# Kernel tuning notes

Hardware: AMD Instinct MI355X
Metric: run time of the kernel (lower is better)

## Reference

```python
import jax, jax.numpy as jnp
import numpy as np

N_NODES = 50000


def _gcn_edges(edge_index, n):
    # add self loops, then symmetric GCN normalization D^-1/2 (A+I) D^-1/2
    loop = jnp.arange(n, dtype=edge_index.dtype)
    src = jnp.concatenate([edge_index[0], loop])
    dst = jnp.concatenate([edge_index[1], loop])
    deg = jax.ops.segment_sum(jnp.ones_like(src, dtype=jnp.float32), dst, num_segments=n)
    dinv = jnp.where(deg > 0, jax.lax.rsqrt(deg), 0.0)
    norm = dinv[src] * dinv[dst]
    return src, dst, norm


def _encoder(x, edge_index, w1, b1, w2, b2, w3, b3, n):
    src, dst, norm = _gcn_edges(edge_index, n)

    def prop(h):
        # sparse spmm: scatter-add of normalized gathered source features
        return jax.ops.segment_sum(h[src] * norm[:, None], dst, num_segments=n)

    def layer(h, w, b):
        # powers [0,1,2]: incrementally apply adjacency, linear per power, concat
        outs, cur = [], h
        for p in range(w.shape[0]):
            if p > 0:
                cur = prop(cur)
            outs.append(cur @ w[p] + b[p])
        return jnp.tanh(jnp.concatenate(outs, axis=-1))

    h = layer(x, w1, b1)
    h = layer(h, w2, b2)
    return layer(h, w3, b3)


def setup_inputs() -> dict:
    key = jax.random.key(0)
    ks = jax.random.split(key, 16)
    n, e, d = N_NODES, 800000, 256
    inp = {
        "x": jax.random.normal(ks[0], (n, d), dtype=jnp.float32),
        "edge_index": jax.random.randint(ks[1], (2, e), 0, n, dtype=jnp.int64),
    }
    dims = [(d, 64), (192, 64), (192, 64)]
    i = 2
    for enc in ("out", "in"):
        for li, (din, dout) in enumerate(dims, start=1):
            s = 1.0 / np.sqrt(din)
            inp[f"w{enc}{li}"] = jax.random.uniform(ks[i], (3, din, dout), jnp.float32, -s, s); i += 1
            inp[f"b{enc}{li}"] = jax.random.uniform(ks[i], (3, dout), jnp.float32, -s, s); i += 1
    return inp


def reference(x, edge_index, wout1, bout1, wout2, bout2, wout3, bout3,
              win1, bin1, win2, bin2, win3, bin3):
    n = x.shape[0]
    zout = _encoder(x, edge_index, wout1, bout1, wout2, bout2, wout3, bout3, n)
    zin = _encoder(x, edge_index[::-1], win1, bin1, win2, bin2, win3, bin3, n)
    return (zout, zin)
```

## Files before the change

### kernel.cpp

```cpp
#include <hip/hip_runtime.h>
#include <hip/hip_bf16.h>

#define NN 50000
#define EE 800000
#define NTILES 782
#define NB 391

typedef __bf16 bf16x8 __attribute__((ext_vector_type(8)));
typedef unsigned short us8 __attribute__((ext_vector_type(8)));
typedef float f32x4 __attribute__((ext_vector_type(4)));

__device__ __forceinline__ unsigned short f2bf(float f) {
  unsigned u = __float_as_uint(f);
  u += 0x7FFFu + ((u >> 16) & 1u);
  return (unsigned short)(u >> 16);
}
__device__ __forceinline__ float bflo(unsigned u) { return __uint_as_float(u << 16); }
__device__ __forceinline__ float bfhi(unsigned u) { return __uint_as_float(u & 0xFFFF0000u); }
__device__ __forceinline__ float bf2f(unsigned short h) { return __uint_as_float(((unsigned)h) << 16); }
__device__ __forceinline__ float fast_tanh(float x) {
  float e = __expf(2.0f * x);
  return 1.0f - 2.0f / (e + 1.0f);
}


__global__ __launch_bounds__(256) void k_hist(const int* __restrict__ ei, int* __restrict__ bCnt) {
  __shared__ int h[2 * NB];
  for (int i = threadIdx.x; i < 2 * NB; i += 256) h[i] = 0;
  __syncthreads();
  int base = blockIdx.x * 2048;
#pragma unroll
  for (int j = 0; j < 8; ++j) {
    int e = base + j * 256 + threadIdx.x;
    if (e < EE) {
      int s = ei[e], d = ei[EE + e];
      atomicAdd(&h[d >> 7], 1);
      atomicAdd(&h[NB + (s >> 7)], 1);
    }
  }
  __syncthreads();
  for (int i = threadIdx.x; i < 2 * NB; i += 256) {
    int c = h[i];
    if (c) atomicAdd(&bCnt[i], c);
  }
}

__global__ __launch_bounds__(512) void k_bscan(const int* __restrict__ bCnt,
                                               int* __restrict__ bOff, int* __restrict__ bCur) {
  __shared__ int sd[512];
  int z = blockIdx.x, t = threadIdx.x;
  sd[t] = (t < NB) ? bCnt[z * NB + t] : 0;
  __syncthreads();
  for (int o = 1; o < 512; o <<= 1) {
    int v = (t >= o) ? sd[t - o] : 0;
    __syncthreads();
    sd[t] += v;
    __syncthreads();
  }
  int ex = (t > 0) ? sd[t - 1] : 0;
  if (t < NB) { bOff[z * (NB + 1) + t] = ex; bCur[z * NB + t] = ex; }
  if (t == NB) bOff[z * (NB + 1) + NB] = ex;
}

__global__ __launch_bounds__(256) void k_scatter(const int* __restrict__ ei,
                                                 int* __restrict__ bCur,
                                                 unsigned* __restrict__ binA,
                                                 unsigned* __restrict__ binB) {
  __shared__ int h[2 * NB];
  for (int i = threadIdx.x; i < 2 * NB; i += 256) h[i] = 0;
  __syncthreads();
  int base = blockIdx.x * 2048;
  int s[8], d[8], la[8], lb[8];
#pragma unroll
  for (int j = 0; j < 8; ++j) {
    int e = base + j * 256 + threadIdx.x;
    d[j] = -1;
    if (e < EE) {
      s[j] = ei[e]; d[j] = ei[EE + e];
      la[j] = atomicAdd(&h[d[j] >> 7], 1);
      lb[j] = atomicAdd(&h[NB + (s[j] >> 7)], 1);
    }
  }
  __syncthreads();
  for (int i = threadIdx.x; i < 2 * NB; i += 256) {
    int c = h[i];
    if (c) h[i] = atomicAdd(&bCur[i], c);
  }
  __syncthreads();
#pragma unroll
  for (int j = 0; j < 8; ++j) {
    if (d[j] >= 0) {
      int pa = h[d[j] >> 7] + la[j];
      binA[pa] = ((unsigned)s[j] << 7) | (unsigned)(d[j] & 127);
      int pb = h[NB + (s[j] >> 7)] + lb[j];
      binB[pb] = ((unsigned)d[j] << 7) | (unsigned)(s[j] & 127);
    }
  }
}

__global__ __launch_bounds__(256) void k_build(const unsigned* __restrict__ binA,
                                               const unsigned* __restrict__ binB,
                                               const int* __restrict__ bOff,
                                               int* __restrict__ rpA, int* __restrict__ rpB,
                                               int* __restrict__ colA, int* __restrict__ colB,
                                               float* __restrict__ dinvA, float* __restrict__ dinvB) {
  int z = blockIdx.y, b = blockIdx.x, t = threadIdx.x;
  const unsigned* bin = z ? binB : binA;
  int* rp = z ? rpB : rpA;
  int* col = z ? colB : colA;
  float* dinv = z ? dinvB : dinvA;

  int e0 = bOff[z * (NB + 1) + b], e1 = bOff[z * (NB + 1) + b + 1];

  __shared__ int cnt[128];
  __shared__ int scn[128];
  __shared__ int cur[128];
  if (t < 128) cnt[t] = 0;
  __syncthreads();
  for (int e = e0 + t; e < e1; e += 256) atomicAdd(&cnt[bin[e] & 127], 1);
  __syncthreads();
  if (t < 128) scn[t] = cnt[t];
  __syncthreads();
  for (int o = 1; o < 128; o <<= 1) {
    int v = (t < 128 && t >= o) ? scn[t - o] : 0;
    __syncthreads();
    if (t < 128) scn[t] += v;
    __syncthreads();
  }
  if (t < 128) {
    int ex = scn[t] - cnt[t];
    cur[t] = ex;
    int node = b * 128 + t;
    if (node <= NN) rp[node] = e0 + ex;
    if (node < NN) dinv[node] = rsqrtf((float)(cnt[t] + 1));
  }
  if (b == 0 && t < 8) col[EE + t] = 0;
  __syncthreads();
  for (int e = e0 + t; e < e1; e += 256) {
    unsigned p = bin[e];
    int pos = e0 + atomicAdd(&cur[p & 127], 1);
    col[pos] = (int)(p >> 7);
  }
}


template<int K, bool F32IN>
__global__ __launch_bounds__(256) void k_gemm(const void* __restrict__ in0, const void* __restrict__ in1,
                                              const float* __restrict__ W0, const float* __restrict__ W1,
                                              const float* __restrict__ dinvA, const float* __restrict__ dinvB,
                                              unsigned short* __restrict__ Z0, unsigned short* __restrict__ Z1) {
  constexpr int KS = K / 32;
  constexpr int KP = K + 8;
  __shared__ unsigned short A_lds[64 * KP];
  __shared__ float dvt[64];

  int z = blockIdx.y;
  const void* Ain = z ? in1 : in0;
  const float* W = z ? W1 : W0;
  const float* dinv = z ? dinvB : dinvA;
  unsigned short* Zo = z ? Z1 : Z0;

  int t = threadIdx.x;
  int lane = t & 63, wv = t >> 6;
  int nloc = lane & 15, quad = lane >> 4;

  bf16x8 b[3][KS];
#pragma unroll
  for (int nt = 0; nt < 3; ++nt) {
    int ncol = wv * 48 + nt * 16 + nloc;
    const float* wp = W + (ncol >> 6) * (K * 64) + (ncol & 63);
#pragma unroll
    for (int ks = 0; ks < KS; ++ks) {
      int kb = ks * 32 + quad * 8;
      us8 u;
#pragma unroll
      for (int i = 0; i < 8; ++i) u[i] = f2bf(wp[(kb + i) * 64]);
      b[nt][ks] = __builtin_bit_cast(bf16x8, u);
    }
  }

  for (int bm = blockIdx.x; bm < NTILES; bm += gridDim.x) {
    int m0 = bm * 64;
    __syncthreads();
    if (t < 64) dvt[t] = (m0 + t < NN) ? dinv[m0 + t] : 0.f;
#pragma unroll
    for (int it = 0; it < KS; ++it) {
      int c = it * 256 + t;
      int row = c / (K / 8);
      int kc  = c % (K / 8);
      int gr = m0 + row;
      us8 val;
      if (F32IN) {
        float4 v0 = make_float4(0, 0, 0, 0), v1 = make_float4(0, 0, 0, 0);
        if (gr < NN) {
          const float* Af = (const float*)Ain + (size_t)gr * K + kc * 8;
          v0 = *(const float4*)(Af);
          v1 = *(const float4*)(Af + 4);
        }
        val[0] = f2bf(v0.x); val[1] = f2bf(v0.y); val[2] = f2bf(v0.z); val[3] = f2bf(v0.w);
        val[4] = f2bf(v1.x); val[5] = f2bf(v1.y); val[6] = f2bf(v1.z); val[7] = f2bf(v1.w);
      } else {
        if (gr < NN) val = *(const us8*)((const unsigned short*)Ain + (size_t)gr * K + kc * 8);
        else         val = (us8)0;
      }
      *(us8*)(&A_lds[row * KP + kc * 8]) = val;
    }
    __syncthreads();

    f32x4 acc[4][3];
#pragma unroll
    for (int mt = 0; mt < 4; ++mt)
#pragma unroll
      for (int nt = 0; nt < 3; ++nt) acc[mt][nt] = (f32x4){0.f, 0.f, 0.f, 0.f};

#pragma unroll
    for (int ks = 0; ks < KS; ++ks) {
      bf16x8 a[4];
#pragma unroll
      for (int mt = 0; mt < 4; ++mt)
        a[mt] = *(const bf16x8*)(&A_lds[(mt * 16 + nloc) * KP + ks * 32 + quad * 8]);
#pragma unroll
      for (int mt = 0; mt < 4; ++mt)
#pragma unroll
        for (int nt = 0; nt < 3; ++nt)
          acc[mt][nt] = __builtin_amdgcn_mfma_f32_16x16x32_bf16(a[mt], b[nt][ks], acc[mt][nt], 0, 0, 0);
    }

#pragma unroll
    for (int mt = 0; mt < 4; ++mt) {
      int rowb = m0 + mt * 16 + quad * 4;
#pragma unroll
      for (int nt = 0; nt < 3; ++nt) {
        int colg = wv * 48 + nt * 16 + nloc;
        bool sc = (wv * 48 + nt * 16) >= 64;
#pragma unroll
        for (int r = 0; r < 4; ++r) {
          int rr = rowb + r;
          float scale = sc ? dvt[mt * 16 + quad * 4 + r] : 1.0f;
          if (rr < NN) Zo[(size_t)rr * 192 + colg] = f2bf(acc[mt][nt][r] * scale);
        }
      }
    }
  }
}


__global__ __launch_bounds__(256) void k_prop1(const unsigned short* __restrict__ Z0,
                                               const unsigned short* __restrict__ Z1,
                                               unsigned short* __restrict__ T0,
                                               unsigned short* __restrict__ T1,
                                               const int* __restrict__ rpA, const int* __restrict__ rpB,
                                               const int* __restrict__ colA, const int* __restrict__ colB,
                                               const float* __restrict__ dinvA, const float* __restrict__ dinvB) {
  int z = blockIdx.y;
  const unsigned short* Z = z ? Z1 : Z0;
  unsigned short* T = z ? T1 : T0;
  const int* rp = z ? rpB : rpA;
  const int* col = z ? colB : colA;
  const float* dinv = z ? dinvB : dinvA;

  int wv = threadIdx.x >> 6, lane = threadIdx.x & 63;
  int v = blockIdx.x * 4 + wv;
  v = __builtin_amdgcn_readfirstlane(v);

  int e0 = rp[v], e1 = rp[v + 1];
  float dv = dinv[v];

  unsigned selfv = ((const unsigned*)(Z + (size_t)v * 192 + 64))[lane];
  float ax = bflo(selfv), ay = bfhi(selfv);

  int e = e0;
  if (e + 8 <= e1) {
    int idx[8];
#pragma unroll
    for (int j = 0; j < 8; ++j) idx[j] = col[e + j];
    e += 8;
    for (; e + 8 <= e1; e += 8) {
      int nidx[8];
#pragma unroll
      for (int j = 0; j < 8; ++j) nidx[j] = col[e + j];
      unsigned pp[8];
#pragma unroll
      for (int j = 0; j < 8; ++j) pp[j] = ((const unsigned*)(Z + (size_t)idx[j] * 192 + 64))[lane];
#pragma unroll
      for (int j = 0; j < 8; ++j) { ax += bflo(pp[j]); ay += bfhi(pp[j]); }
#pragma unroll
      for (int j = 0; j < 8; ++j) idx[j] = nidx[j];
    }
    unsigned pp[8];
#pragma unroll
    for (int j = 0; j < 8; ++j) pp[j] = ((const unsigned*)(Z + (size_t)idx[j] * 192 + 64))[lane];
#pragma unroll
    for (int j = 0; j < 8; ++j) { ax += bflo(pp[j]); ay += bfhi(pp[j]); }
  }
  int r = e1 - e;
  if (r > 0) {
    int idx[8];
#pragma unroll
    for (int j = 0; j < 8; ++j) idx[j] = col[e + j];
    unsigned pp[8];
#pragma unroll
    for (int j = 0; j < 8; ++j) pp[j] = ((const unsigned*)(Z + (size_t)idx[j] * 192 + 64))[lane];
#pragma unroll
    for (int j = 0; j < 8; ++j) if (j < r) { ax += bflo(pp[j]); ay += bfhi(pp[j]); }
  }

  ax *= dv; ay *= dv;
  float sc = (lane >= 32) ? dv : 1.0f;
  unsigned o = (unsigned)f2bf(ax * sc) | ((unsigned)f2bf(ay * sc) << 16);
  ((unsigned*)(T + (size_t)v * 128))[lane] = o;
}


template<bool FINAL>
__global__ __launch_bounds__(256) void k_combine(const unsigned short* __restrict__ Z0,
                                                 const unsigned short* __restrict__ Z1,
                                                 const unsigned short* __restrict__ T0,
                                                 const unsigned short* __restrict__ T1,
                                                 unsigned short* __restrict__ H0,
                                                 unsigned short* __restrict__ H1,
                                                 float* __restrict__ out,
                                                 const float* __restrict__ bia0, const float* __restrict__ bia1,
                                                 const int* __restrict__ rpA, const int* __restrict__ rpB,
                                                 const int* __restrict__ colA, const int* __restrict__ colB,
                                                 const float* __restrict__ dinvA, const float* __restrict__ dinvB) {
  int z = blockIdx.y;
  const unsigned short* Z = z ? Z1 : Z0;
  const unsigned short* T = z ? T1 : T0;
  unsigned short* H = z ? H1 : H0;
  const float* bias = z ? bia1 : bia0;
  const int* rp = z ? rpB : rpA;
  const int* col = z ? colB : colA;
  const float* dinv = z ? dinvB : dinvA;

  int wv = threadIdx.x >> 6, lane = threadIdx.x & 63;
  int v = blockIdx.x * 4 + wv;
  v = __builtin_amdgcn_readfirstlane(v);

  int e0 = rp[v], e1 = rp[v + 1];
  float dv = dinv[v];

  const unsigned short* Trow = T + (size_t)v * 128;
  float u = bf2f(Trow[64 + lane]);

  int e = e0;
  if (e + 8 <= e1) {
    int idx[8];
#pragma unroll
    for (int j = 0; j < 8; ++j) idx[j] = col[e + j];
    e += 8;
    for (; e + 8 <= e1; e += 8) {
      int nidx[8];
#pragma unroll
      for (int j = 0; j < 8; ++j) nidx[j] = col[e + j];
      float pp[8];
#pragma unroll
      for (int j = 0; j < 8; ++j) pp[j] = bf2f(T[(size_t)idx[j] * 128 + 64 + lane]);
#pragma unroll
      for (int j = 0; j < 8; ++j) u += pp[j];
#pragma unroll
      for (int j = 0; j < 8; ++j) idx[j] = nidx[j];
    }
    float pp[8];
#pragma unroll
    for (int j = 0; j < 8; ++j) pp[j] = bf2f(T[(size_t)idx[j] * 128 + 64 + lane]);
#pragma unroll
    for (int j = 0; j < 8; ++j) u += pp[j];
  }
  int r = e1 - e;
  if (r > 0) {
    int idx[8];
#pragma unroll
    for (int j = 0; j < 8; ++j) idx[j] = col[e + j];
    float pp[8];
#pragma unroll
    for (int j = 0; j < 8; ++j) pp[j] = bf2f(T[(size_t)idx[j] * 128 + 64 + lane]);
#pragma unroll
    for (int j = 0; j < 8; ++j) if (j < r) u += pp[j];
  }
  u *= dv;

  float p0 = fast_tanh(bf2f(Z[(size_t)v * 192 + lane]) + bias[lane]);
  float p1 = fast_tanh(bf2f(Trow[lane]) + bias[64 + lane]);
  float p2 = fast_tanh(u + bias[128 + lane]);

  if (FINAL) {
    float* o = out + (size_t)z * NN * 192 + (size_t)v * 192;
    o[lane] = p0; o[lane + 64] = p1; o[lane + 128] = p2;
  } else {
    unsigned short* h = H + (size_t)v * 192;
    h[lane] = f2bf(p0); h[lane + 64] = f2bf(p1); h[lane + 128] = f2bf(p2);
  }
}


extern "C" void kernel_launch(void* const* d_in, const int* in_sizes, int n_in,
                              void* d_out, int out_size, void* d_ws, size_t ws_size,
                              hipStream_t stream) {
  const float* x  = (const float*)d_in[0];
  const int* ei   = (const int*)d_in[1];
  const float* wout1 = (const float*)d_in[2];
  const float* bout1 = (const float*)d_in[3];
  const float* wout2 = (const float*)d_in[4];
  const float* bout2 = (const float*)d_in[5];
  const float* wout3 = (const float*)d_in[6];
  const float* bout3 = (const float*)d_in[7];
  const float* win1  = (const float*)d_in[8];
  const float* bin1  = (const float*)d_in[9];
  const float* win2  = (const float*)d_in[10];
  const float* bin2  = (const float*)d_in[11];
  const float* win3  = (const float*)d_in[12];
  const float* bin3  = (const float*)d_in[13];
  float* out = (float*)d_out;

  char* p = (char*)d_ws;
  auto alloc = [&](size_t bytes) { char* r = p; p += (bytes + 255) & ~(size_t)255; return r; };
  int* rpA   = (int*)alloc((size_t)(NN + 1) * 4);
  int* rpB   = (int*)alloc((size_t)(NN + 1) * 4);
  int* colA  = (int*)alloc((size_t)(EE + 8) * 4);
  int* colB  = (int*)alloc((size_t)(EE + 8) * 4);
  float* dinvA = (float*)alloc((size_t)NN * 4);
  float* dinvB = (float*)alloc((size_t)NN * 4);
  int* bCnt  = (int*)alloc((size_t)2 * NB * 4);
  int* bOff  = (int*)alloc((size_t)2 * (NB + 1) * 4);
  int* bCur  = (int*)alloc((size_t)2 * NB * 4);
  unsigned short* Z0 = (unsigned short*)alloc((size_t)NN * 192 * 2);
  unsigned short* Z1 = (unsigned short*)alloc((size_t)NN * 192 * 2);
  unsigned short* T0 = (unsigned short*)alloc((size_t)NN * 128 * 2);
  unsigned short* T1 = (unsigned short*)alloc((size_t)NN * 128 * 2);
  unsigned short* H0 = (unsigned short*)alloc((size_t)NN * 192 * 2);
  unsigned short* H1 = (unsigned short*)alloc((size_t)NN * 192 * 2);

  unsigned* binA = (unsigned*)Z0;
  unsigned* binB = (unsigned*)Z1;

  hipMemsetAsync(bCnt, 0, (size_t)2 * NB * 4, stream);
  k_hist<<<391, 256, 0, stream>>>(ei, bCnt);
  k_bscan<<<2, 512, 0, stream>>>(bCnt, bOff, bCur);
  k_scatter<<<391, 256, 0, stream>>>(ei, bCur, binA, binB);
  k_build<<<dim3(NB, 2), 256, 0, stream>>>(binA, binB, bOff, rpA, rpB, colA, colB, dinvA, dinvB);

  dim3 gGemm(196, 2);
  dim3 gProp(12500, 2);

  k_gemm<256, true><<<gGemm, 256, 0, stream>>>(x, x, wout1, win1, dinvA, dinvB, Z0, Z1);
  k_prop1<<<gProp, 256, 0, stream>>>(Z0, Z1, T0, T1, rpA, rpB, colA, colB, dinvA, dinvB);
  k_combine<false><<<gProp, 256, 0, stream>>>(Z0, Z1, T0, T1, H0, H1, nullptr, bout1, bin1,
                                              rpA, rpB, colA, colB, dinvA, dinvB);
  k_gemm<192, false><<<gGemm, 256, 0, stream>>>(H0, H1, wout2, win2, dinvA, dinvB, Z0, Z1);
  k_prop1<<<gProp, 256, 0, stream>>>(Z0, Z1, T0, T1, rpA, rpB, colA, colB, dinvA, dinvB);
  k_combine<false><<<gProp, 256, 0, stream>>>(Z0, Z1, T0, T1, H0, H1, nullptr, bout2, bin2,
                                              rpA, rpB, colA, colB, dinvA, dinvB);
  k_gemm<192, false><<<gGemm, 256, 0, stream>>>(H0, H1, wout3, win3, dinvA, dinvB, Z0, Z1);
  k_prop1<<<gProp, 256, 0, stream>>>(Z0, Z1, T0, T1, rpA, rpB, colA, colB, dinvA, dinvB);
  k_combine<true><<<gProp, 256, 0, stream>>>(Z0, Z1, T0, T1, H0, H1, out, bout3, bin3,
                                             rpA, rpB, colA, colB, dinvA, dinvB);
}
```

Baseline: 565.4 us.

## Prepack bf16 weights and split edges across half-waves in propagation gathers

Adds a kernel that converts and transposes all six weight tensors to bf16 once, so each GEMM block loads its B fragments with vector loads instead of strided scalar fp32 loads plus conversion. The GEMM grid doubles to 391 blocks per encoder. The two propagation kernels now have each half-wave handle alternate edges with wider per-lane loads (8 or 4 bytes), then combine the halves with cross-lane shuffles. This issues fewer, wider gather requests per edge, at the cost of extra shuffles and a larger column padding.

```diff
diff --git a/kernel.cpp b/kernel.cpp
--- a/kernel.cpp
+++ b/kernel.cpp
@@ -21,6 +21,24 @@
 __device__ __forceinline__ float fast_tanh(float x) {
   float e = __expf(2.0f * x);
   return 1.0f - 2.0f / (e + 1.0f);
+}
+
+
+__global__ __launch_bounds__(256) void k_pack(const float* __restrict__ w0, const float* __restrict__ w1,
+                                              const float* __restrict__ w2, const float* __restrict__ w3,
+                                              const float* __restrict__ w4, const float* __restrict__ w5,
+                                              unsigned short* t0, unsigned short* t1,
+                                              unsigned short* t2, unsigned short* t3,
+                                              unsigned short* t4, unsigned short* t5) {
+  int y = blockIdx.y;
+  const float* W = (y == 0) ? w0 : (y == 1) ? w1 : (y == 2) ? w2 : (y == 3) ? w3 : (y == 4) ? w4 : w5;
+  unsigned short* T = (y == 0) ? t0 : (y == 1) ? t1 : (y == 2) ? t2 : (y == 3) ? t3 : (y == 4) ? t4 : t5;
+  int K = (y < 2) ? 256 : 192;
+  int tid = blockIdx.x * 256 + threadIdx.x;
+  if (tid >= 192 * K) return;
+  int col = tid / K;
+  int k = tid - col * K;
+  T[tid] = f2bf(W[(col >> 6) * (K * 64) + k * 64 + (col & 63)]);
 }
 
 
@@ -134,7 +152,7 @@
     if (node <= NN) rp[node] = e0 + ex;
     if (node < NN) dinv[node] = rsqrtf((float)(cnt[t] + 1));
   }
-  if (b == 0 && t < 8) col[EE + t] = 0;
+  if (b == 0 && t < 16) col[EE + t] = 0;
   __syncthreads();
   for (int e = e0 + t; e < e1; e += 256) {
     unsigned p = bin[e];
@@ -146,7 +164,8 @@
 
 template<int K, bool F32IN>
 __global__ __launch_bounds__(256) void k_gemm(const void* __restrict__ in0, const void* __restrict__ in1,
-                                              const float* __restrict__ W0, const float* __restrict__ W1,
+                                              const unsigned short* __restrict__ Wt0,
+                                              const unsigned short* __restrict__ Wt1,
                                               const float* __restrict__ dinvA, const float* __restrict__ dinvB,
                                               unsigned short* __restrict__ Z0, unsigned short* __restrict__ Z1) {
   constexpr int KS = K / 32;
@@ -156,7 +175,7 @@
 
   int z = blockIdx.y;
   const void* Ain = z ? in1 : in0;
-  const float* W = z ? W1 : W0;
+  const unsigned short* Wt = z ? Wt1 : Wt0;
   const float* dinv = z ? dinvB : dinvA;
   unsigned short* Zo = z ? Z1 : Z0;
 
@@ -168,15 +187,9 @@
 #pragma unroll
   for (int nt = 0; nt < 3; ++nt) {
     int ncol = wv * 48 + nt * 16 + nloc;
-    const float* wp = W + (ncol >> 6) * (K * 64) + (ncol & 63);
-#pragma unroll
-    for (int ks = 0; ks < KS; ++ks) {
-      int kb = ks * 32 + quad * 8;
-      us8 u;
-#pragma unroll
-      for (int i = 0; i < 8; ++i) u[i] = f2bf(wp[(kb + i) * 64]);
-      b[nt][ks] = __builtin_bit_cast(bf16x8, u);
-    }
+#pragma unroll
+    for (int ks = 0; ks < KS; ++ks)
+      b[nt][ks] = *(const bf16x8*)(Wt + (size_t)ncol * K + ks * 32 + quad * 8);
   }
 
   for (int bm = blockIdx.x; bm < NTILES; bm += gridDim.x) {
@@ -260,55 +273,73 @@
   const float* dinv = z ? dinvB : dinvA;
 
   int wv = threadIdx.x >> 6, lane = threadIdx.x & 63;
-  int v = blockIdx.x * 4 + wv;
-  v = __builtin_amdgcn_readfirstlane(v);
+  int h = lane >> 5, l = lane & 31;
+  int v = __builtin_amdgcn_readfirstlane(blockIdx.x * 4 + wv);
 
   int e0 = rp[v], e1 = rp[v + 1];
   float dv = dinv[v];
 
-  unsigned selfv = ((const unsigned*)(Z + (size_t)v * 192 + 64))[lane];
-  float ax = bflo(selfv), ay = bfhi(selfv);
+  float a0 = 0, a1 = 0, a2 = 0, a3 = 0;
 
   int e = e0;
-  if (e + 8 <= e1) {
+  if (e + 16 <= e1) {
     int idx[8];
 #pragma unroll
-    for (int j = 0; j < 8; ++j) idx[j] = col[e + j];
-    e += 8;
-    for (; e + 8 <= e1; e += 8) {
+    for (int j = 0; j < 8; ++j) idx[j] = col[e + 2 * j + h];
+    e += 16;
+    while (e + 16 <= e1) {
       int nidx[8];
 #pragma unroll
-      for (int j = 0; j < 8; ++j) nidx[j] = col[e + j];
-      unsigned pp[8];
-#pragma unroll
-      for (int j = 0; j < 8; ++j) pp[j] = ((const unsigned*)(Z + (size_t)idx[j] * 192 + 64))[lane];
-#pragma unroll
-      for (int j = 0; j < 8; ++j) { ax += bflo(pp[j]); ay += bfhi(pp[j]); }
+      for (int j = 0; j < 8; ++j) nidx[j] = col[e + 2 * j + h];
+      uint2 pp[8];
+#pragma unroll
+      for (int j = 0; j < 8; ++j) pp[j] = *(const uint2*)(Z + (size_t)idx[j] * 192 + 64 + l * 4);
+#pragma unroll
+      for (int j = 0; j < 8; ++j) {
+        a0 += bflo(pp[j].x); a1 += bfhi(pp[j].x);
+        a2 += bflo(pp[j].y); a3 += bfhi(pp[j].y);
+      }
 #pragma unroll
       for (int j = 0; j < 8; ++j) idx[j] = nidx[j];
-    }
-    unsigned pp[8];
-#pragma unroll
-    for (int j = 0; j < 8; ++j) pp[j] = ((const unsigned*)(Z + (size_t)idx[j] * 192 + 64))[lane];
-#pragma unroll
-    for (int j = 0; j < 8; ++j) { ax += bflo(pp[j]); ay += bfhi(pp[j]); }
+      e += 16;
+    }
+    uint2 pp[8];
+#pragma unroll
+    for (int j = 0; j < 8; ++j) pp[j] = *(const uint2*)(Z + (size_t)idx[j] * 192 + 64 + l * 4);
+#pragma unroll
+    for (int j = 0; j < 8; ++j) {
+      a0 += bflo(pp[j].x); a1 += bfhi(pp[j].x);
+      a2 += bflo(pp[j].y); a3 += bfhi(pp[j].y);
+    }
   }
   int r = e1 - e;
   if (r > 0) {
     int idx[8];
 #pragma unroll
-    for (int j = 0; j < 8; ++j) idx[j] = col[e + j];
-    unsigned pp[8];
-#pragma unroll
-    for (int j = 0; j < 8; ++j) pp[j] = ((const unsigned*)(Z + (size_t)idx[j] * 192 + 64))[lane];
-#pragma unroll
-    for (int j = 0; j < 8; ++j) if (j < r) { ax += bflo(pp[j]); ay += bfhi(pp[j]); }
-  }
-
-  ax *= dv; ay *= dv;
-  float sc = (lane >= 32) ? dv : 1.0f;
-  unsigned o = (unsigned)f2bf(ax * sc) | ((unsigned)f2bf(ay * sc) << 16);
-  ((unsigned*)(T + (size_t)v * 128))[lane] = o;
+    for (int j = 0; j < 8; ++j) idx[j] = col[e + 2 * j + h];
+    uint2 pp[8];
+#pragma unroll
+    for (int j = 0; j < 8; ++j) pp[j] = *(const uint2*)(Z + (size_t)idx[j] * 192 + 64 + l * 4);
+#pragma unroll
+    for (int j = 0; j < 8; ++j) if (2 * j + h < r) {
+      a0 += bflo(pp[j].x); a1 += bfhi(pp[j].x);
+      a2 += bflo(pp[j].y); a3 += bfhi(pp[j].y);
+    }
+  }
+
+  a0 += __shfl_xor(a0, 32); a1 += __shfl_xor(a1, 32);
+  a2 += __shfl_xor(a2, 32); a3 += __shfl_xor(a3, 32);
+
+  uint2 sv = *(const uint2*)(Z + (size_t)v * 192 + 64 + l * 4);
+  a0 += bflo(sv.x); a1 += bfhi(sv.x); a2 += bflo(sv.y); a3 += bfhi(sv.y);
+
+  float sc = dv * (l >= 16 ? dv : 1.0f);
+  if (h == 0) {
+    uint2 o;
+    o.x = (unsigned)f2bf(a0 * sc) | ((unsigned)f2bf(a1 * sc) << 16);
+    o.y = (unsigned)f2bf(a2 * sc) | ((unsigned)f2bf(a3 * sc) << 16);
+    *(uint2*)(T + (size_t)v * 128 + l * 4) = o;
+  }
 }
 
 
@@ -334,50 +365,59 @@
   const float* dinv = z ? dinvB : dinvA;
 
   int wv = threadIdx.x >> 6, lane = threadIdx.x & 63;
-  int v = blockIdx.x * 4 + wv;
-  v = __builtin_amdgcn_readfirstlane(v);
+  int h = lane >> 5, l = lane & 31;
+  int v = __builtin_amdgcn_readfirstlane(blockIdx.x * 4 + wv);
 
   int e0 = rp[v], e1 = rp[v + 1];
   float dv = dinv[v];
 
-  const unsigned short* Trow = T + (size_t)v * 128;
-  float u = bf2f(Trow[64 + lane]);
+  float u0 = 0, u1 = 0;
 
   int e = e0;
-  if (e + 8 <= e1) {
+  if (e + 16 <= e1) {
     int idx[8];
 #pragma unroll
-    for (int j = 0; j < 8; ++j) idx[j] = col[e + j];
-    e += 8;
-    for (; e + 8 <= e1; e += 8) {
+    for (int j = 0; j < 8; ++j) idx[j] = col[e + 2 * j + h];
+    e += 16;
+    while (e + 16 <= e1) {
       int nidx[8];
 #pragma unroll
-      for (int j = 0; j < 8; ++j) nidx[j] = col[e + j];
-      float pp[8];
-#pragma unroll
-      for (int j = 0; j < 8; ++j) pp[j] = bf2f(T[(size_t)idx[j] * 128 + 64 + lane]);
-#pragma unroll
-      for (int j = 0; j < 8; ++j) u += pp[j];
+      for (int j = 0; j < 8; ++j) nidx[j] = col[e + 2 * j + h];
+      unsigned pp[8];
+#pragma unroll
+      for (int j = 0; j < 8; ++j) pp[j] = *(const unsigned*)(T + (size_t)idx[j] * 128 + 64 + l * 2);
+#pragma unroll
+      for (int j = 0; j < 8; ++j) { u0 += bflo(pp[j]); u1 += bfhi(pp[j]); }
 #pragma unroll
       for (int j = 0; j < 8; ++j) idx[j] = nidx[j];
-    }
-    float pp[8];
-#pragma unroll
-    for (int j = 0; j < 8; ++j) pp[j] = bf2f(T[(size_t)idx[j] * 128 + 64 + lane]);
-#pragma unroll
-    for (int j = 0; j < 8; ++j) u += pp[j];
+      e += 16;
+    }
+    unsigned pp[8];
+#pragma unroll
+    for (int j = 0; j < 8; ++j) pp[j] = *(const unsigned*)(T + (size_t)idx[j] * 128 + 64 + l * 2);
+#pragma unroll
+    for (int j = 0; j < 8; ++j) { u0 += bflo(pp[j]); u1 += bfhi(pp[j]); }
   }
   int r = e1 - e;
   if (r > 0) {
     int idx[8];
 #pragma unroll
-    for (int j = 0; j < 8; ++j) idx[j] = col[e + j];
-    float pp[8];
-#pragma unroll
-    for (int j = 0; j < 8; ++j) pp[j] = bf2f(T[(size_t)idx[j] * 128 + 64 + lane]);
-#pragma unroll
-    for (int j = 0; j < 8; ++j) if (j < r) u += pp[j];
-  }
+    for (int j = 0; j < 8; ++j) idx[j] = col[e + 2 * j + h];
+    unsigned pp[8];
+#pragma unroll
+    for (int j = 0; j < 8; ++j) pp[j] = *(const unsigned*)(T + (size_t)idx[j] * 128 + 64 + l * 2);
+#pragma unroll
+    for (int j = 0; j < 8; ++j) if (2 * j + h < r) { u0 += bflo(pp[j]); u1 += bfhi(pp[j]); }
+  }
+
+  u0 += __shfl_xor(u0, 32);
+  u1 += __shfl_xor(u1, 32);
+  float ua = __shfl(u0, lane >> 1);
+  float ub = __shfl(u1, lane >> 1);
+  float u = (lane & 1) ? ub : ua;
+
+  const unsigned short* Trow = T + (size_t)v * 128;
+  u += bf2f(Trow[64 + lane]);
   u *= dv;
 
   float p0 = fast_tanh(bf2f(Z[(size_t)v * 192 + lane]) + bias[lane]);
@@ -388,8 +428,8 @@
     float* o = out + (size_t)z * NN * 192 + (size_t)v * 192;
     o[lane] = p0; o[lane + 64] = p1; o[lane + 128] = p2;
   } else {
-    unsigned short* h = H + (size_t)v * 192;
-    h[lane] = f2bf(p0); h[lane + 64] = f2bf(p1); h[lane + 128] = f2bf(p2);
+    unsigned short* hh = H + (size_t)v * 192;
+    hh[lane] = f2bf(p0); hh[lane + 64] = f2bf(p1); hh[lane + 128] = f2bf(p2);
   }
 }
 
@@ -417,13 +457,19 @@
   auto alloc = [&](size_t bytes) { char* r = p; p += (bytes + 255) & ~(size_t)255; return r; };
   int* rpA   = (int*)alloc((size_t)(NN + 1) * 4);
   int* rpB   = (int*)alloc((size_t)(NN + 1) * 4);
-  int* colA  = (int*)alloc((size_t)(EE + 8) * 4);
-  int* colB  = (int*)alloc((size_t)(EE + 8) * 4);
+  int* colA  = (int*)alloc((size_t)(EE + 16) * 4);
+  int* colB  = (int*)alloc((size_t)(EE + 16) * 4);
   float* dinvA = (float*)alloc((size_t)NN * 4);
   float* dinvB = (float*)alloc((size_t)NN * 4);
   int* bCnt  = (int*)alloc((size_t)2 * NB * 4);
   int* bOff  = (int*)alloc((size_t)2 * (NB + 1) * 4);
   int* bCur  = (int*)alloc((size_t)2 * NB * 4);
+  unsigned short* wt0 = (unsigned short*)alloc((size_t)192 * 256 * 2);
+  unsigned short* wt1 = (unsigned short*)alloc((size_t)192 * 256 * 2);
+  unsigned short* wt2 = (unsigned short*)alloc((size_t)192 * 192 * 2);
+  unsigned short* wt3 = (unsigned short*)alloc((size_t)192 * 192 * 2);
+  unsigned short* wt4 = (unsigned short*)alloc((size_t)192 * 192 * 2);
+  unsigned short* wt5 = (unsigned short*)alloc((size_t)192 * 192 * 2);
   unsigned short* Z0 = (unsigned short*)alloc((size_t)NN * 192 * 2);
   unsigned short* Z1 = (unsigned short*)alloc((size_t)NN * 192 * 2);
   unsigned short* T0 = (unsigned short*)alloc((size_t)NN * 128 * 2);
@@ -434,24 +480,26 @@
   unsigned* binA = (unsigned*)Z0;
   unsigned* binB = (unsigned*)Z1;
 
+  k_pack<<<dim3(192, 6), 256, 0, stream>>>(wout1, win1, wout2, win2, wout3, win3,
+                                           wt0, wt1, wt2, wt3, wt4, wt5);
   hipMemsetAsync(bCnt, 0, (size_t)2 * NB * 4, stream);
   k_hist<<<391, 256, 0, stream>>>(ei, bCnt);
   k_bscan<<<2, 512, 0, stream>>>(bCnt, bOff, bCur);
   k_scatter<<<391, 256, 0, stream>>>(ei, bCur, binA, binB);
   k_build<<<dim3(NB, 2), 256, 0, stream>>>(binA, binB, bOff, rpA, rpB, colA, colB, dinvA, dinvB);
 
-  dim3 gGemm(196, 2);
+  dim3 gGemm(391, 2);
   dim3 gProp(12500, 2);
 
-  k_gemm<256, true><<<gGemm, 256, 0, stream>>>(x, x, wout1, win1, dinvA, dinvB, Z0, Z1);
+  k_gemm<256, true><<<gGemm, 256, 0, stream>>>(x, x, wt0, wt1, dinvA, dinvB, Z0, Z1);
   k_prop1<<<gProp, 256, 0, stream>>>(Z0, Z1, T0, T1, rpA, rpB, colA, colB, dinvA, dinvB);
   k_combine<false><<<gProp, 256, 0, stream>>>(Z0, Z1, T0, T1, H0, H1, nullptr, bout1, bin1,
                                               rpA, rpB, colA, colB, dinvA, dinvB);
-  k_gemm<192, false><<<gGemm, 256, 0, stream>>>(H0, H1, wout2, win2, dinvA, dinvB, Z0, Z1);
+  k_gemm<192, false><<<gGemm, 256, 0, stream>>>(H0, H1, wt2, wt3, dinvA, dinvB, Z0, Z1);
   k_prop1<<<gProp, 256, 0, stream>>>(Z0, Z1, T0, T1, rpA, rpB, colA, colB, dinvA, dinvB);
   k_combine<false><<<gProp, 256, 0, stream>>>(Z0, Z1, T0, T1, H0, H1, nullptr, bout2, bin2,
                                               rpA, rpB, colA, colB, dinvA, dinvB);
-  k_gemm<192, false><<<gGemm, 256, 0, stream>>>(H0, H1, wout3, win3, dinvA, dinvB, Z0, Z1);
+  k_gemm<192, false><<<gGemm, 256, 0, stream>>>(H0, H1, wt4, wt5, dinvA, dinvB, Z0, Z1);
   k_prop1<<<gProp, 256, 0, stream>>>(Z0, Z1, T0, T1, rpA, rpB, colA, colB, dinvA, dinvB);
   k_combine<true><<<gProp, 256, 0, stream>>>(Z0, Z1, T0, T1, H0, H1, out, bout3, bin3,
                                              rpA, rpB, colA, colB, dinvA, dinvB);
```

After: 590.7 us. 1.04x slower.
